# Kernel tuning notes

Hardware: AMD Instinct MI355X
Metric: run time of the kernel (lower is better)

Reference implementation:

```python
import jax, jax.numpy as jnp
import numpy as np
import math

B, S, D, H = 1, 4096, 1024, 16
DH = D // H


def setup_inputs() -> dict:
    key = jax.random.key(0)
    k1, k2, k3 = jax.random.split(key, 3)
    x = jax.random.normal(k1, (B, S, D), dtype=jnp.float32)
    # additive causal mask: 0 where allowed, -1e9 where masked (future)
    causal = jnp.tril(jnp.ones((S, S), dtype=bool))
    mask = jnp.where(causal, 0.0, -1e9).astype(jnp.float32)[None]  # [1,S,S]
    W_attn = jax.random.normal(k2, (D, 3 * D), dtype=jnp.float32) * 0.02
    b_attn = jnp.zeros((3 * D,), dtype=jnp.float32)
    W_proj = jax.random.normal(k3, (D, D), dtype=jnp.float32) * 0.02
    b_proj = jnp.zeros((D,), dtype=jnp.float32)
    return {"x": x, "mask": mask, "W_attn": W_attn, "b_attn": b_attn,
            "W_proj": W_proj, "b_proj": b_proj}


def reference(x, mask, W_attn, b_attn, W_proj, b_proj):
    # c_attn: fused QKV projection
    qkv = x @ W_attn + b_attn                      # [B,S,3D]
    q, k, v = jnp.split(qkv, 3, axis=-1)           # each [B,S,D]

    def heads(t):  # [B,S,D] -> [B,H,S,DH]
        return t.reshape(B, S, H, DH).transpose(0, 2, 1, 3)

    q, k, v = heads(q), heads(k), heads(v)
    # scores: eager O(S^2) matrix as in original
    w = jnp.einsum('bhqd,bhkd->bhqk', q, k) / math.sqrt(DH)
    w = w + mask[:, None, :, :]                    # broadcast over heads
    w = jax.nn.softmax(w, axis=-1)                 # dropout p=0 -> identity
    a = jnp.einsum('bhqk,bhkd->bhqd', w, v)        # [B,H,S,DH]
    a = a.transpose(0, 2, 1, 3).reshape(B, S, D)   # merge heads
    return a @ W_proj + b_proj
```

## Files before the change

### kernel.cpp

```cpp
#include <hip/hip_runtime.h>

typedef _Float16 half8 __attribute__((ext_vector_type(8)));
typedef short short8 __attribute__((ext_vector_type(8)));
typedef float floatx4 __attribute__((ext_vector_type(4)));

static __device__ __forceinline__ float bf2f(unsigned short u) {
  union { unsigned int u; float f; } c; c.u = ((unsigned int)u) << 16; return c.f;
}
static __device__ __forceinline__ unsigned short f2bf(float f) {
  union { float f; unsigned int u; } c; c.f = f;
  return (unsigned short)((c.u + 0x7fffu + ((c.u >> 16) & 1u)) >> 16);
}
static __device__ __forceinline__ unsigned short f2h(float f) {
  union { _Float16 h; unsigned short u; } c; c.h = (_Float16)f; return c.u;
}
static __device__ __forceinline__ unsigned int cvtpk(float a, float b) {
  unsigned int r;
  asm("v_cvt_pk_bf16_f32 %0, %1, %2" : "=v"(r) : "v"(a), "v"(b));
  return r;
}

#define GL2LDS16(gsrc, ldst)                                                        \
  __builtin_amdgcn_global_load_lds(                                                 \
      (const __attribute__((address_space(1))) void*)(const void*)(gsrc),           \
      (__attribute__((address_space(3))) void*)(void*)(ldst), 16, 0, 0)

static __device__ __forceinline__ int dtype_bf16(const unsigned short* mask16) {
  return mask16[1] != 0;
}

__global__ __launch_bounds__(256) void k_prep(const void* __restrict__ x,
    const void* __restrict__ Wa, const void* __restrict__ Wp,
    const unsigned short* __restrict__ mask16, _Float16* __restrict__ xh,
    _Float16* __restrict__ WaT, _Float16* __restrict__ WpT) {
  __shared__ float tile[64 * 65];
  const int dt = dtype_bf16(mask16);
  const int bx = blockIdx.x;
  const int tid = threadIdx.x;
  if (bx < 4096) {
    const int i = (bx * 256 + tid) * 4;
    _Float16 o[4];
    if (dt) {
      ushort4 u = *((const ushort4*)((const unsigned short*)x + i));
      o[0] = (_Float16)bf2f(u.x); o[1] = (_Float16)bf2f(u.y);
      o[2] = (_Float16)bf2f(u.z); o[3] = (_Float16)bf2f(u.w);
    } else {
      float4 f = *((const float4*)((const float*)x + i));
      o[0] = (_Float16)f.x; o[1] = (_Float16)f.y;
      o[2] = (_Float16)f.z; o[3] = (_Float16)f.w;
    }
    union { _Float16 h[4]; uint2 u; } pk;
    pk.h[0] = o[0]; pk.h[1] = o[1]; pk.h[2] = o[2]; pk.h[3] = o[3];
    *((uint2*)(xh + i)) = pk.u;
    return;
  }
  const void* in; _Float16* out; int n0, k0, N;
  if (bx < 4864) { const int b = bx - 4096; in = Wa; out = WaT; N = 3072;
                   n0 = (b % 48) * 64; k0 = (b / 48) * 64; }
  else           { const int b = bx - 4864; in = Wp; out = WpT; N = 1024;
                   n0 = (b % 16) * 64; k0 = (b / 16) * 64; }
  const int r = tid >> 2;
#pragma unroll
  for (int it = 0; it < 4; ++it) {
    const int c4 = (tid & 3) + it * 4;
    const size_t src = (size_t)(k0 + r) * N + n0 + c4 * 4;
    float v[4];
    if (dt) {
      ushort4 u = *((const ushort4*)((const unsigned short*)in + src));
      v[0] = bf2f(u.x); v[1] = bf2f(u.y); v[2] = bf2f(u.z); v[3] = bf2f(u.w);
    } else {
      float4 f = *((const float4*)((const float*)in + src));
      v[0] = f.x; v[1] = f.y; v[2] = f.z; v[3] = f.w;
    }
#pragma unroll
    for (int jj = 0; jj < 4; ++jj) tile[r * 65 + c4 * 4 + jj] = v[jj];
  }
  __syncthreads();
#pragma unroll
  for (int it = 0; it < 4; ++it) {
    const int rn = (tid >> 4) + it * 16;
    const int kc = tid & 15;
    union { _Float16 h[4]; uint2 u; } pk;
#pragma unroll
    for (int jj = 0; jj < 4; ++jj)
      pk.h[jj] = (_Float16)tile[(kc * 4 + jj) * 65 + rn];
    *(uint2*)(out + (size_t)(n0 + rn) * 1024 + k0 + kc * 4) = pk.u;
  }
}

template <int KD>
static __device__ __forceinline__ void gemm_mainloop(const _Float16* __restrict__ A,
    const _Float16* __restrict__ Bt, int m0, int n0,
    _Float16* As, _Float16* Bs, floatx4 acc[4][4]) {
  const int tid = threadIdx.x;
  const int wave = tid >> 6, lane = tid & 63;
  const int lq = lane & 15, quad = lane >> 4;
  const int wm = (wave >> 1) * 64, wn = (wave & 1) * 64;
  const int scol = (lane & 3) * 8;
  for (int k0 = 0; k0 < KD; k0 += 32) {
    __syncthreads();
#pragma unroll
    for (int op = 0; op < 2; ++op) {
      const int rbase = wave * 32 + op * 16;
      const int row = rbase + (lane >> 2);
      GL2LDS16(A + (size_t)(m0 + row) * KD + k0 + scol, As + rbase * 32);
      GL2LDS16(Bt + (size_t)(n0 + row) * KD + k0 + scol, Bs + rbase * 32);
    }
    __builtin_amdgcn_s_waitcnt(0x0f70);
    __syncthreads();
    half8 af[4], bf[4];
#pragma unroll
    for (int i = 0; i < 4; ++i) {
      af[i] = *(const half8*)(As + (wm + i * 16 + lq) * 32 + quad * 8);
      bf[i] = *(const half8*)(Bs + (wn + i * 16 + lq) * 32 + quad * 8);
    }
#pragma unroll
    for (int i = 0; i < 4; ++i)
#pragma unroll
      for (int j = 0; j < 4; ++j)
        acc[i][j] = __builtin_amdgcn_mfma_f32_16x16x32_f16(af[i], bf[j], acc[i][j], 0, 0, 0);
  }
}

__global__ __launch_bounds__(256, 1) void k_gemm_qkv(const _Float16* __restrict__ A,
    const _Float16* __restrict__ Bt, const void* __restrict__ bias,
    const unsigned short* __restrict__ mask16, _Float16* __restrict__ Qb,
    _Float16* __restrict__ Kb, unsigned short* __restrict__ VTb) {
  __shared__ __attribute__((aligned(16))) unsigned short smem[128 * 136];
  _Float16* As = (_Float16*)smem;
  _Float16* Bs = As + 4096;
  const int tid = threadIdx.x, wave = tid >> 6, lane = tid & 63;
  const int lq = lane & 15, quad = lane >> 4;
  const int m0 = blockIdx.y * 128, n0 = blockIdx.x * 128;
  const int wm = (wave >> 1) * 64, wn = (wave & 1) * 64;
  floatx4 acc[4][4] = {};
  gemm_mainloop<1024>(A, Bt, m0, n0, As, Bs, acc);
  const int dt = dtype_bf16(mask16);
  const int sec = n0 >> 10;
  const float scale = (sec == 0) ? 0.1803368801f : 1.0f;
  __syncthreads();
#pragma unroll
  for (int i = 0; i < 4; ++i) {
    const int lmb = wm + i * 16 + quad * 4;
#pragma unroll
    for (int j = 0; j < 4; ++j) {
      const int ln = wn + j * 16 + lq;
      const int gcol = n0 + ln;
      const float bv = dt ? bf2f(((const unsigned short*)bias)[gcol])
                          : ((const float*)bias)[gcol];
#pragma unroll
      for (int r = 0; r < 4; ++r) {
        const float v = (acc[i][j][r] + bv) * scale;
        const unsigned short bits = (sec == 2) ? f2bf(v) : f2h(v);
        if (sec == 2) smem[ln * 136 + lmb + r] = bits;
        else          smem[(lmb + r) * 136 + ln] = bits;
      }
    }
  }
  __syncthreads();
  if (sec == 2) {
#pragma unroll
    for (int it = 0; it < 8; ++it) {
      const int row = (tid >> 4) + it * 16;
      const int ch = tid & 15;
      const uint4 v = *(const uint4*)&smem[row * 136 + ch * 8];
      *(uint4*)(VTb + (size_t)(n0 + row - 2048) * 4096 + m0 + ch * 8) = v;
    }
  } else {
    _Float16* dst = (sec == 0) ? Qb : Kb;
#pragma unroll
    for (int it = 0; it < 8; ++it) {
      const int row = (tid >> 4) + it * 16;
      const int ch = tid & 15;
      const uint4 v = *(const uint4*)&smem[row * 136 + ch * 8];
      const int c = (n0 & 1023) + ch * 8;
      const int hh = c >> 6, dh = c & 63;
      *(uint4*)(dst + ((size_t)(hh * 4096 + m0 + row)) * 64 + dh) = v;
    }
  }
}

__global__ __launch_bounds__(256, 2) void k_attn(const _Float16* __restrict__ Qb,
    const _Float16* __restrict__ Kb, const unsigned short* __restrict__ VTb,
    unsigned short* __restrict__ Op0, unsigned short* __restrict__ Op1,
    unsigned short* __restrict__ Op2, unsigned short* __restrict__ Op3,
    float* __restrict__ Lp) {
  constexpr int S = 4096;
  const int bx = blockIdx.x;
  const int h  = bx & 15;
  const int pr = (bx >> 4) & 7;
  const int cj = bx >> 7;
  const int kbg = 15 - pr;
  const int ksm = pr;
  const int sB  = 64 - 4 * pr;
  const int fb  = sB / 17;
  const int p0 = cj * 17, p1 = p0 + 17;
  const int tid = threadIdx.x, wave = tid >> 6, lane = tid & 63;
  const int lq = lane & 15, quad = lane >> 4;
  __shared__ __attribute__((aligned(16))) _Float16 Ks[64 * 72];
  __shared__ __attribute__((aligned(16))) unsigned short VTs[64 * 72];
  const _Float16* Qh = Qb + (size_t)h * S * 64;
  const _Float16* Kh = Kb + (size_t)h * S * 64;
  const unsigned short* VTh = VTb + (size_t)h * 64 * S;
  short8 aones;
#pragma unroll
  for (int jj = 0; jj < 8; ++jj) aones[jj] = (short)0x3F80;
  const int srow = tid >> 2, schunk = (tid & 3) * 16;

#define LOADQ()                                                                     \
  {                                                                                 \
    const int qb0 = 256 * ku + wave * 64;                                           \
    _Pragma("unroll")                                                               \
    for (int m = 0; m < 4; ++m)                                                     \
      _Pragma("unroll")                                                             \
      for (int ch = 0; ch < 2; ++ch)                                                \
        qf[m][ch] = *(const half8*)(Qh + (size_t)(qb0 + m * 16 + lq) * 64           \
                                    + ch * 32 + quad * 8);                          \
  }
#define ZEROACC()                                                                   \
  {                                                                                 \
    _Pragma("unroll")                                                               \
    for (int nf = 0; nf < 4; ++nf)                                                  \
      _Pragma("unroll")                                                             \
      for (int m = 0; m < 4; ++m) o[nf][m] = (floatx4){0.f, 0.f, 0.f, 0.f};         \
    _Pragma("unroll")                                                               \
    for (int m = 0; m < 4; ++m) ol[m] = (floatx4){0.f, 0.f, 0.f, 0.f};              \
  }
#define EPILOGUE(SLOT)                                                              \
  {                                                                                 \
    const int sl = (SLOT);                                                          \
    unsigned short* Ob = sl == 0 ? Op0 : sl == 1 ? Op1 : sl == 2 ? Op2 : Op3;       \
    const int r0 = sl << 10;                                                        \
    const int qb0 = 256 * ku + wave * 64;                                           \
    _Pragma("unroll")                                                               \
    for (int m = 0; m < 4; ++m) {                                                   \
      const int q = qb0 + m * 16 + lq;                                              \
      _Pragma("unroll")                                                             \
      for (int nf = 0; nf < 4; ++nf) {                                              \
        union { unsigned short u[4]; uint2 v; } pk;                                 \
        _Pragma("unroll")                                                           \
        for (int r = 0; r < 4; ++r) pk.u[r] = f2bf(o[nf][m][r]);                    \
        *(uint2*)(Ob + (size_t)(q - r0) * 1024 + h * 64 + nf * 16 + quad * 4) =     \
            pk.v;                                                                   \
      }                                                                             \
      if (quad == 0) Lp[sl * 65536 + h * 4096 + q] = ol[m][0];                      \
    }                                                                               \
  }

  int ku = (p0 < sB) ? kbg : ksm;
  half8 qf[4][2];
  floatx4 o[4][4];
  floatx4 ol[4];
  LOADQ();
  ZEROACC();
  uint4 kreg0, kreg1, vreg0, vreg1;
  {
    const int t0 = (p0 < sB) ? p0 : p0 - sB;
    const int kt = t0 * 64;
    kreg0 = *(const uint4*)(Kh + (size_t)(kt + srow) * 64 + schunk);
    kreg1 = *(const uint4*)(Kh + (size_t)(kt + srow) * 64 + schunk + 8);
    vreg0 = *(const uint4*)(VTh + (size_t)srow * S + kt + schunk);
    vreg1 = *(const uint4*)(VTh + (size_t)srow * S + kt + schunk + 8);
  }
  for (int pos = p0; pos < p1; ++pos) {
    if (pos == sB) {
      EPILOGUE(cj);
      ku = ksm;
      LOADQ();
      ZEROACC();
    }
    const int t = (pos < sB) ? pos : pos - sB;
    const int kt = t * 64;
    __syncthreads();
    *(uint4*)(Ks + srow * 72 + schunk) = kreg0;
    *(uint4*)(Ks + srow * 72 + schunk + 8) = kreg1;
    *(uint4*)(VTs + srow * 72 + schunk) = vreg0;
    *(uint4*)(VTs + srow * 72 + schunk + 8) = vreg1;
    __syncthreads();
    if (pos + 1 < p1) {
      const int nx = pos + 1;
      const int tn = (nx < sB) ? nx : nx - sB;
      const int kn = tn * 64;
      kreg0 = *(const uint4*)(Kh + (size_t)(kn + srow) * 64 + schunk);
      kreg1 = *(const uint4*)(Kh + (size_t)(kn + srow) * 64 + schunk + 8);
      vreg0 = *(const uint4*)(VTh + (size_t)srow * S + kn + schunk);
      vreg1 = *(const uint4*)(VTh + (size_t)srow * S + kn + schunk + 8);
    }
    const int qb0 = 256 * ku + wave * 64;
    if ((wave >= 2) || (t < 4 * ku + 2)) {
#pragma unroll
      for (int c = 0; c < 2; ++c) {
        floatx4 sc[4][2];
        {
          half8 kf0[2], kf1[2];
#pragma unroll
          for (int kb = 0; kb < 2; ++kb) {
            const int row = (c * 2 + kb) * 16 + lq;
            kf0[kb] = *(const half8*)(Ks + row * 72 + quad * 8);
            kf1[kb] = *(const half8*)(Ks + row * 72 + 32 + quad * 8);
          }
#pragma unroll
          for (int m = 0; m < 4; ++m)
#pragma unroll
            for (int kb = 0; kb < 2; ++kb) {
              floatx4 z = {0.f, 0.f, 0.f, 0.f};
              z = __builtin_amdgcn_mfma_f32_16x16x32_f16(kf0[kb], qf[m][0], z, 0, 0, 0);
              sc[m][kb] = __builtin_amdgcn_mfma_f32_16x16x32_f16(kf1[kb], qf[m][1], z, 0, 0, 0);
            }
        }
        short8 pf[4];
#pragma unroll
        for (int m = 0; m < 4; ++m) {
          unsigned int dw0, dw1, dw2, dw3;
          if (kt + c * 32 + 31 > qb0 + m * 16) {
            const int q = qb0 + m * 16 + lq;
            float pv0[4], pv1[4];
#pragma unroll
            for (int r = 0; r < 4; ++r) {
              const int key0 = kt + (c * 2 + 0) * 16 + quad * 4 + r;
              const int key1 = kt + (c * 2 + 1) * 16 + quad * 4 + r;
              const float e0 = __builtin_amdgcn_exp2f(sc[m][0][r]);
              const float e1 = __builtin_amdgcn_exp2f(sc[m][1][r]);
              pv0[r] = (key0 > q) ? 0.f : e0;
              pv1[r] = (key1 > q) ? 0.f : e1;
            }
            dw0 = cvtpk(pv0[0], pv0[1]); dw1 = cvtpk(pv0[2], pv0[3]);
            dw2 = cvtpk(pv1[0], pv1[1]); dw3 = cvtpk(pv1[2], pv1[3]);
          } else {
            float pv0[4], pv1[4];
#pragma unroll
            for (int r = 0; r < 4; ++r) {
              pv0[r] = __builtin_amdgcn_exp2f(sc[m][0][r]);
              pv1[r] = __builtin_amdgcn_exp2f(sc[m][1][r]);
            }
            dw0 = cvtpk(pv0[0], pv0[1]); dw1 = cvtpk(pv0[2], pv0[3]);
            dw2 = cvtpk(pv1[0], pv1[1]); dw3 = cvtpk(pv1[2], pv1[3]);
          }
          asm("v_permlane32_swap_b32 %0, %1" : "+v"(dw0), "+v"(dw2));
          asm("v_permlane32_swap_b32 %0, %1" : "+v"(dw1), "+v"(dw3));
          asm("v_permlane16_swap_b32 %0, %1" : "+v"(dw0), "+v"(dw2));
          asm("v_permlane16_swap_b32 %0, %1" : "+v"(dw1), "+v"(dw3));
          union { unsigned int d[4]; short8 s; } u;
          u.d[0] = dw0; u.d[1] = dw1; u.d[2] = dw2; u.d[3] = dw3;
          pf[m] = u.s;
        }
#pragma unroll
        for (int nf = 0; nf < 4; ++nf) {
          const short8 vfr = *(const short8*)(VTs + (nf * 16 + lq) * 72 + c * 32 + quad * 8);
#pragma unroll
          for (int m = 0; m < 4; ++m)
            o[nf][m] = __builtin_amdgcn_mfma_f32_16x16x32_bf16(vfr, pf[m], o[nf][m], 0, 0, 0);
        }
#pragma unroll
        for (int m = 0; m < 4; ++m)
          ol[m] = __builtin_amdgcn_mfma_f32_16x16x32_bf16(aones, pf[m], ol[m], 0, 0, 0);
      }
    }
  }
  EPILOGUE((p1 <= sB) ? cj : cj - fb);
#undef LOADQ
#undef ZEROACC
#undef EPILOGUE
}

__global__ __launch_bounds__(256) void k_merge(const unsigned short* __restrict__ Op0,
    const unsigned short* __restrict__ Op1, const unsigned short* __restrict__ Op2,
    const unsigned short* __restrict__ Op3, const float* __restrict__ Lp,
    _Float16* __restrict__ Ah) {
  const int row = blockIdx.x;
  const int c = threadIdx.x * 4;
  const int h = c >> 6;
  const int k = row >> 8;
  const int n = (k >= 8) ? (4 * k + 20) / 17 : 4 - (64 - 4 * k) / 17;
  float l = 0.f, v0 = 0.f, v1 = 0.f, v2 = 0.f, v3 = 0.f;
#pragma unroll
  for (int s = 0; s < 4; ++s) {
    if (s < n) {
      const unsigned short* Ob = s == 0 ? Op0 : s == 1 ? Op1 : s == 2 ? Op2 : Op3;
      l += Lp[s * 65536 + h * 4096 + row];
      const ushort4 a = *(const ushort4*)(Ob + (size_t)(row - (s << 10)) * 1024 + c);
      v0 += bf2f(a.x); v1 += bf2f(a.y); v2 += bf2f(a.z); v3 += bf2f(a.w);
    }
  }
  const float inv = __builtin_amdgcn_rcpf(l);
  union { _Float16 h4[4]; uint2 u; } pk;
  pk.h4[0] = (_Float16)(v0 * inv);
  pk.h4[1] = (_Float16)(v1 * inv);
  pk.h4[2] = (_Float16)(v2 * inv);
  pk.h4[3] = (_Float16)(v3 * inv);
  *(uint2*)(Ah + (size_t)row * 1024 + c) = pk.u;
}

__global__ __launch_bounds__(256, 1) void k_gemm_proj(const _Float16* __restrict__ A,
    const _Float16* __restrict__ Bt, const void* __restrict__ bias,
    const unsigned short* __restrict__ mask16, void* __restrict__ out) {
  __shared__ __attribute__((aligned(16))) _Float16 As[64 * 32];
  __shared__ __attribute__((aligned(16))) _Float16 Bs[128 * 32];
  const int tid = threadIdx.x, wave = tid >> 6, lane = tid & 63;
  const int lq = lane & 15, quad = lane >> 4;
  const int m0 = blockIdx.y * 64, n0 = blockIdx.x * 128;
  const int wm = (wave >> 1) * 32, wn = (wave & 1) * 64;
  const int scol = (lane & 3) * 8;
  floatx4 acc[2][4] = {};
  for (int k0 = 0; k0 < 1024; k0 += 32) {
    __syncthreads();
    {
      const int arow = wave * 16 + (lane >> 2);
      GL2LDS16(A + (size_t)(m0 + arow) * 1024 + k0 + scol, As + wave * 16 * 32);
#pragma unroll
      for (int op = 0; op < 2; ++op) {
        const int rbase = wave * 32 + op * 16;
        const int row = rbase + (lane >> 2);
        GL2LDS16(Bt + (size_t)(n0 + row) * 1024 + k0 + scol, Bs + rbase * 32);
      }
    }
    __builtin_amdgcn_s_waitcnt(0x0f70);
    __syncthreads();
    half8 af[2], bf[4];
#pragma unroll
    for (int i = 0; i < 2; ++i)
      af[i] = *(const half8*)(As + (wm + i * 16 + lq) * 32 + quad * 8);
#pragma unroll
    for (int j = 0; j < 4; ++j)
      bf[j] = *(const half8*)(Bs + (wn + j * 16 + lq) * 32 + quad * 8);
#pragma unroll
    for (int i = 0; i < 2; ++i)
#pragma unroll
      for (int j = 0; j < 4; ++j)
        acc[i][j] = __builtin_amdgcn_mfma_f32_16x16x32_f16(af[i], bf[j], acc[i][j], 0, 0, 0);
  }
  const int dt = dtype_bf16(mask16);
#pragma unroll
  for (int i = 0; i < 2; ++i) {
    const int growb = m0 + wm + i * 16 + quad * 4;
#pragma unroll
    for (int j = 0; j < 4; ++j) {
      const int gcol = n0 + wn + j * 16 + lq;
      const float bv = dt ? bf2f(((const unsigned short*)bias)[gcol])
                          : ((const float*)bias)[gcol];
#pragma unroll
      for (int r = 0; r < 4; ++r) {
        const float v = acc[i][j][r] + bv;
        if (dt) ((unsigned short*)out)[(size_t)(growb + r) * 1024 + gcol] = f2bf(v);
        else    ((float*)out)[(size_t)(growb + r) * 1024 + gcol] = v;
      }
    }
  }
}

extern "C" void kernel_launch(void* const* d_in, const int* in_sizes, int n_in,
                              void* d_out, int out_size, void* d_ws, size_t ws_size,
                              hipStream_t stream) {
  const void* x    = d_in[0];
  const unsigned short* mask16 = (const unsigned short*)d_in[1];
  const void* Wa   = d_in[2];
  const void* ba   = d_in[3];
  const void* Wp   = d_in[4];
  const void* bp   = d_in[5];
  char* ws = (char*)d_ws;
  _Float16* WpT       = (_Float16*)(ws + 0);
  _Float16* WaT       = (_Float16*)(ws + 2097152);
  float*    Lp        = (float*)   (ws + 2097152);
  unsigned short* Op2 = (unsigned short*)(ws + 3145728);
  _Float16* xh        = (_Float16*)(ws + 8388608);
  unsigned short* Op0 = (unsigned short*)(ws + 8388608);
  _Float16* Qb        = (_Float16*)(ws + 16777216);
  _Float16* Ah        = (_Float16*)(ws + 16777216);
  _Float16* Kb        = (_Float16*)(ws + 25165824);
  unsigned short* VTb = (unsigned short*)(ws + 33554432);
  unsigned short* Op1 = (unsigned short*)(ws + 41943040);
  unsigned short* Op3 = (unsigned short*)(ws + 48234496);

  k_prep<<<5120, 256, 0, stream>>>(x, Wa, Wp, mask16, xh, WaT, WpT);
  { dim3 g(24, 32); k_gemm_qkv<<<g, 256, 0, stream>>>(xh, WaT, ba, mask16, Qb, Kb, VTb); }
  k_attn<<<512, 256, 0, stream>>>(Qb, Kb, VTb, Op0, Op1, Op2, Op3, Lp);
  k_merge<<<4096, 256, 0, stream>>>(Op0, Op1, Op2, Op3, Lp, Ah);
  { dim3 g(8, 64);  k_gemm_proj<<<g, 256, 0, stream>>>(Ah, WpT, bp, mask16, d_out); }
}
```

Measured before the change: 240.6 us.

## Double-buffer K/V tiles via async global-to-LDS loads with XOR swizzle

Replaces the register-staged K/V prefetch (global load into registers, then LDS store between two barriers) with direct global_load_lds into a double-buffered LDS tile, so the next tile streams in while the current one is computed. Padding is replaced by an XOR swizzle to avoid bank conflicts, and s_setprio raises wave priority around the MFMA blocks. This removes one barrier per iteration and the register round-trip. In exchange it doubles LDS use, which may limit occupancy, and relies on a full vmcnt wait at the end of each iteration.

```diff
diff --git a/kernel.cpp b/kernel.cpp
--- a/kernel.cpp
+++ b/kernel.cpp
@@ -197,16 +197,30 @@
   const int p0 = cj * 17, p1 = p0 + 17;
   const int tid = threadIdx.x, wave = tid >> 6, lane = tid & 63;
   const int lq = lane & 15, quad = lane >> 4;
-  __shared__ __attribute__((aligned(16))) _Float16 Ks[64 * 72];
-  __shared__ __attribute__((aligned(16))) unsigned short VTs[64 * 72];
+  __shared__ __attribute__((aligned(16))) _Float16 Ks[2][64 * 64];
+  __shared__ __attribute__((aligned(16))) unsigned short VTs[2][64 * 64];
   const _Float16* Qh = Qb + (size_t)h * S * 64;
   const _Float16* Kh = Kb + (size_t)h * S * 64;
   const unsigned short* VTh = VTb + (size_t)h * 64 * S;
   short8 aones;
 #pragma unroll
   for (int jj = 0; jj < 8; ++jj) aones[jj] = (short)0x3F80;
-  const int srow = tid >> 2, schunk = (tid & 3) * 16;
-
+  const int srow8 = lane >> 3;
+  const int swch  = ((lane & 7) ^ srow8) * 8;
+  const int rowKV = wave * 16 + srow8;
+  const int sdst  = wave * 1024 + lane * 8;
+  const int xr = lq & 7;
+
+#define STAGE(BUF, KT)                                                              \
+  {                                                                                 \
+    _Pragma("unroll")                                                               \
+    for (int j = 0; j < 2; ++j) {                                                   \
+      GL2LDS16(Kh + (size_t)((KT) + rowKV + j * 8) * 64 + swch,                     \
+               &Ks[BUF][wave * 1024 + j * 512]);                                    \
+      GL2LDS16(VTh + (size_t)(rowKV + j * 8) * S + (KT) + swch,                     \
+               &VTs[BUF][wave * 1024 + j * 512]);                                   \
+    }                                                                               \
+  }
 #define LOADQ()                                                                     \
   {                                                                                 \
     const int qb0 = 256 * ku + wave * 64;                                           \
@@ -253,39 +267,29 @@
   floatx4 ol[4];
   LOADQ();
   ZEROACC();
-  uint4 kreg0, kreg1, vreg0, vreg1;
   {
     const int t0 = (p0 < sB) ? p0 : p0 - sB;
-    const int kt = t0 * 64;
-    kreg0 = *(const uint4*)(Kh + (size_t)(kt + srow) * 64 + schunk);
-    kreg1 = *(const uint4*)(Kh + (size_t)(kt + srow) * 64 + schunk + 8);
-    vreg0 = *(const uint4*)(VTh + (size_t)srow * S + kt + schunk);
-    vreg1 = *(const uint4*)(VTh + (size_t)srow * S + kt + schunk + 8);
-  }
+    STAGE(0, t0 * 64);
+  }
+  __builtin_amdgcn_s_waitcnt(0x0f70);
+  __syncthreads();
   for (int pos = p0; pos < p1; ++pos) {
+    const int b = (pos - p0) & 1;
     if (pos == sB) {
       EPILOGUE(cj);
       ku = ksm;
       LOADQ();
       ZEROACC();
     }
-    const int t = (pos < sB) ? pos : pos - sB;
-    const int kt = t * 64;
-    __syncthreads();
-    *(uint4*)(Ks + srow * 72 + schunk) = kreg0;
-    *(uint4*)(Ks + srow * 72 + schunk + 8) = kreg1;
-    *(uint4*)(VTs + srow * 72 + schunk) = vreg0;
-    *(uint4*)(VTs + srow * 72 + schunk + 8) = vreg1;
-    __syncthreads();
     if (pos + 1 < p1) {
       const int nx = pos + 1;
       const int tn = (nx < sB) ? nx : nx - sB;
-      const int kn = tn * 64;
-      kreg0 = *(const uint4*)(Kh + (size_t)(kn + srow) * 64 + schunk);
-      kreg1 = *(const uint4*)(Kh + (size_t)(kn + srow) * 64 + schunk + 8);
-      vreg0 = *(const uint4*)(VTh + (size_t)srow * S + kn + schunk);
-      vreg1 = *(const uint4*)(VTh + (size_t)srow * S + kn + schunk + 8);
-    }
+      STAGE(b ^ 1, tn * 64);
+    }
+    const int t = (pos < sB) ? pos : pos - sB;
+    const int kt = t * 64;
+    const _Float16* Ksb = &Ks[b][0];
+    const unsigned short* Vsb = &VTs[b][0];
     const int qb0 = 256 * ku + wave * 64;
     if ((wave >= 2) || (t < 4 * ku + 2)) {
 #pragma unroll
@@ -296,9 +300,10 @@
 #pragma unroll
           for (int kb = 0; kb < 2; ++kb) {
             const int row = (c * 2 + kb) * 16 + lq;
-            kf0[kb] = *(const half8*)(Ks + row * 72 + quad * 8);
-            kf1[kb] = *(const half8*)(Ks + row * 72 + 32 + quad * 8);
+            kf0[kb] = *(const half8*)(Ksb + row * 64 + ((quad ^ xr) << 3));
+            kf1[kb] = *(const half8*)(Ksb + row * 64 + (((quad | 4) ^ xr) << 3));
           }
+          __builtin_amdgcn_s_setprio(1);
 #pragma unroll
           for (int m = 0; m < 4; ++m)
 #pragma unroll
@@ -307,6 +312,7 @@
               z = __builtin_amdgcn_mfma_f32_16x16x32_f16(kf0[kb], qf[m][0], z, 0, 0, 0);
               sc[m][kb] = __builtin_amdgcn_mfma_f32_16x16x32_f16(kf1[kb], qf[m][1], z, 0, 0, 0);
             }
+          __builtin_amdgcn_s_setprio(0);
         }
         short8 pf[4];
 #pragma unroll
@@ -344,9 +350,11 @@
           u.d[0] = dw0; u.d[1] = dw1; u.d[2] = dw2; u.d[3] = dw3;
           pf[m] = u.s;
         }
+        __builtin_amdgcn_s_setprio(1);
 #pragma unroll
         for (int nf = 0; nf < 4; ++nf) {
-          const short8 vfr = *(const short8*)(VTs + (nf * 16 + lq) * 72 + c * 32 + quad * 8);
+          const short8 vfr = *(const short8*)(
+              Vsb + (nf * 16 + lq) * 64 + ((((c << 2) | quad) ^ xr) << 3));
 #pragma unroll
           for (int m = 0; m < 4; ++m)
             o[nf][m] = __builtin_amdgcn_mfma_f32_16x16x32_bf16(vfr, pf[m], o[nf][m], 0, 0, 0);
@@ -354,10 +362,14 @@
 #pragma unroll
         for (int m = 0; m < 4; ++m)
           ol[m] = __builtin_amdgcn_mfma_f32_16x16x32_bf16(aones, pf[m], ol[m], 0, 0, 0);
+        __builtin_amdgcn_s_setprio(0);
       }
     }
+    __builtin_amdgcn_s_waitcnt(0x0f70);
+    __syncthreads();
   }
   EPILOGUE((p1 <= sB) ? cj : cj - fb);
+#undef STAGE
 #undef LOADQ
 #undef ZEROACC
 #undef EPILOGUE
```

Result: no change. 244.1 us (+1.5%).

## Deepen GEMM K-tiles to 64 with XOR-swizzled LDS and XCD-aware block mapping

Applied to the files above, without the earlier changes.

Both GEMM kernels now stage 64-wide K slices per iteration instead of 32. This halves the number of barrier and wait round-trips per tile. LDS rows are XOR-swizzled by row to avoid bank conflicts on the wider 128-byte rows. Launch grids become 1-D, with block IDs remapped so blocks on the same XCD share M rows, aiming for better L2 reuse. The cost is a doubled LDS footprint and more fragment registers per iteration.

```diff
diff --git a/kernel.cpp b/kernel.cpp
--- a/kernel.cpp
+++ b/kernel.cpp
@@ -89,36 +89,41 @@
 }
 
 template <int KD>
-static __device__ __forceinline__ void gemm_mainloop(const _Float16* __restrict__ A,
+static __device__ __forceinline__ void gemm_mainloop64(const _Float16* __restrict__ A,
     const _Float16* __restrict__ Bt, int m0, int n0,
     _Float16* As, _Float16* Bs, floatx4 acc[4][4]) {
   const int tid = threadIdx.x;
   const int wave = tid >> 6, lane = tid & 63;
   const int lq = lane & 15, quad = lane >> 4;
   const int wm = (wave >> 1) * 64, wn = (wave & 1) * 64;
-  const int scol = (lane & 3) * 8;
-  for (int k0 = 0; k0 < KD; k0 += 32) {
+  const int srow8 = lane >> 3;
+  const int swch = ((lane & 7) ^ srow8) * 8;
+  const int xr = lq & 7;
+  for (int k0 = 0; k0 < KD; k0 += 64) {
     __syncthreads();
 #pragma unroll
-    for (int op = 0; op < 2; ++op) {
-      const int rbase = wave * 32 + op * 16;
-      const int row = rbase + (lane >> 2);
-      GL2LDS16(A + (size_t)(m0 + row) * KD + k0 + scol, As + rbase * 32);
-      GL2LDS16(Bt + (size_t)(n0 + row) * KD + k0 + scol, Bs + rbase * 32);
+    for (int op = 0; op < 4; ++op) {
+      const int rb = wave * 32 + op * 8;
+      GL2LDS16(A + (size_t)(m0 + rb + srow8) * KD + k0 + swch, As + rb * 64);
+      GL2LDS16(Bt + (size_t)(n0 + rb + srow8) * KD + k0 + swch, Bs + rb * 64);
     }
     __builtin_amdgcn_s_waitcnt(0x0f70);
     __syncthreads();
-    half8 af[4], bf[4];
-#pragma unroll
-    for (int i = 0; i < 4; ++i) {
-      af[i] = *(const half8*)(As + (wm + i * 16 + lq) * 32 + quad * 8);
-      bf[i] = *(const half8*)(Bs + (wn + i * 16 + lq) * 32 + quad * 8);
-    }
+    half8 af[4][2], bf[4][2];
 #pragma unroll
     for (int i = 0; i < 4; ++i)
 #pragma unroll
-      for (int j = 0; j < 4; ++j)
-        acc[i][j] = __builtin_amdgcn_mfma_f32_16x16x32_f16(af[i], bf[j], acc[i][j], 0, 0, 0);
+      for (int ks = 0; ks < 2; ++ks) {
+        af[i][ks] = *(const half8*)(As + (wm + i * 16 + lq) * 64 + (((ks * 4 + quad) ^ xr) << 3));
+        bf[i][ks] = *(const half8*)(Bs + (wn + i * 16 + lq) * 64 + (((ks * 4 + quad) ^ xr) << 3));
+      }
+#pragma unroll
+    for (int i = 0; i < 4; ++i)
+#pragma unroll
+      for (int j = 0; j < 4; ++j) {
+        acc[i][j] = __builtin_amdgcn_mfma_f32_16x16x32_f16(af[i][0], bf[j][0], acc[i][j], 0, 0, 0);
+        acc[i][j] = __builtin_amdgcn_mfma_f32_16x16x32_f16(af[i][1], bf[j][1], acc[i][j], 0, 0, 0);
+      }
   }
 }
 
@@ -128,13 +133,17 @@
     _Float16* __restrict__ Kb, unsigned short* __restrict__ VTb) {
   __shared__ __attribute__((aligned(16))) unsigned short smem[128 * 136];
   _Float16* As = (_Float16*)smem;
-  _Float16* Bs = As + 4096;
+  _Float16* Bs = As + 8192;
+  const int id = blockIdx.x;
+  const int xcd = id & 7, rr = id >> 3;
+  const int by = xcd * 4 + rr / 24;
+  const int bxn = rr % 24;
   const int tid = threadIdx.x, wave = tid >> 6, lane = tid & 63;
   const int lq = lane & 15, quad = lane >> 4;
-  const int m0 = blockIdx.y * 128, n0 = blockIdx.x * 128;
+  const int m0 = by * 128, n0 = bxn * 128;
   const int wm = (wave >> 1) * 64, wn = (wave & 1) * 64;
   floatx4 acc[4][4] = {};
-  gemm_mainloop<1024>(A, Bt, m0, n0, As, Bs, acc);
+  gemm_mainloop64<1024>(A, Bt, m0, n0, As, Bs, acc);
   const int dt = dtype_bf16(mask16);
   const int sec = n0 >> 10;
   const float scale = (sec == 0) ? 0.1803368801f : 1.0f;
@@ -394,40 +403,52 @@
 __global__ __launch_bounds__(256, 1) void k_gemm_proj(const _Float16* __restrict__ A,
     const _Float16* __restrict__ Bt, const void* __restrict__ bias,
     const unsigned short* __restrict__ mask16, void* __restrict__ out) {
-  __shared__ __attribute__((aligned(16))) _Float16 As[64 * 32];
-  __shared__ __attribute__((aligned(16))) _Float16 Bs[128 * 32];
+  __shared__ __attribute__((aligned(16))) _Float16 As[64 * 64];
+  __shared__ __attribute__((aligned(16))) _Float16 Bs[128 * 64];
+  const int id = blockIdx.x;
+  const int xcd = id & 7, rr = id >> 3;
+  const int by = xcd * 8 + rr / 8;
+  const int bxn = rr % 8;
   const int tid = threadIdx.x, wave = tid >> 6, lane = tid & 63;
   const int lq = lane & 15, quad = lane >> 4;
-  const int m0 = blockIdx.y * 64, n0 = blockIdx.x * 128;
+  const int m0 = by * 64, n0 = bxn * 128;
   const int wm = (wave >> 1) * 32, wn = (wave & 1) * 64;
-  const int scol = (lane & 3) * 8;
+  const int srow8 = lane >> 3;
+  const int swch = ((lane & 7) ^ srow8) * 8;
+  const int xr = lq & 7;
   floatx4 acc[2][4] = {};
-  for (int k0 = 0; k0 < 1024; k0 += 32) {
+  for (int k0 = 0; k0 < 1024; k0 += 64) {
     __syncthreads();
-    {
-      const int arow = wave * 16 + (lane >> 2);
-      GL2LDS16(A + (size_t)(m0 + arow) * 1024 + k0 + scol, As + wave * 16 * 32);
-#pragma unroll
-      for (int op = 0; op < 2; ++op) {
-        const int rbase = wave * 32 + op * 16;
-        const int row = rbase + (lane >> 2);
-        GL2LDS16(Bt + (size_t)(n0 + row) * 1024 + k0 + scol, Bs + rbase * 32);
-      }
+#pragma unroll
+    for (int op = 0; op < 2; ++op) {
+      const int rb = wave * 16 + op * 8;
+      GL2LDS16(A + (size_t)(m0 + rb + srow8) * 1024 + k0 + swch, As + rb * 64);
+    }
+#pragma unroll
+    for (int op = 0; op < 4; ++op) {
+      const int rb = wave * 32 + op * 8;
+      GL2LDS16(Bt + (size_t)(n0 + rb + srow8) * 1024 + k0 + swch, Bs + rb * 64);
     }
     __builtin_amdgcn_s_waitcnt(0x0f70);
     __syncthreads();
-    half8 af[2], bf[4];
+    half8 af[2][2], bf[4][2];
 #pragma unroll
     for (int i = 0; i < 2; ++i)
-      af[i] = *(const half8*)(As + (wm + i * 16 + lq) * 32 + quad * 8);
+#pragma unroll
+      for (int ks = 0; ks < 2; ++ks)
+        af[i][ks] = *(const half8*)(As + (wm + i * 16 + lq) * 64 + (((ks * 4 + quad) ^ xr) << 3));
 #pragma unroll
     for (int j = 0; j < 4; ++j)
-      bf[j] = *(const half8*)(Bs + (wn + j * 16 + lq) * 32 + quad * 8);
+#pragma unroll
+      for (int ks = 0; ks < 2; ++ks)
+        bf[j][ks] = *(const half8*)(Bs + (wn + j * 16 + lq) * 64 + (((ks * 4 + quad) ^ xr) << 3));
 #pragma unroll
     for (int i = 0; i < 2; ++i)
 #pragma unroll
-      for (int j = 0; j < 4; ++j)
-        acc[i][j] = __builtin_amdgcn_mfma_f32_16x16x32_f16(af[i], bf[j], acc[i][j], 0, 0, 0);
+      for (int j = 0; j < 4; ++j) {
+        acc[i][j] = __builtin_amdgcn_mfma_f32_16x16x32_f16(af[i][0], bf[j][0], acc[i][j], 0, 0, 0);
+        acc[i][j] = __builtin_amdgcn_mfma_f32_16x16x32_f16(af[i][1], bf[j][1], acc[i][j], 0, 0, 0);
+      }
   }
   const int dt = dtype_bf16(mask16);
 #pragma unroll
@@ -472,8 +493,8 @@
   unsigned short* Op3 = (unsigned short*)(ws + 48234496);
 
   k_prep<<<5120, 256, 0, stream>>>(x, Wa, Wp, mask16, xh, WaT, WpT);
-  { dim3 g(24, 32); k_gemm_qkv<<<g, 256, 0, stream>>>(xh, WaT, ba, mask16, Qb, Kb, VTb); }
+  k_gemm_qkv<<<768, 256, 0, stream>>>(xh, WaT, ba, mask16, Qb, Kb, VTb);
   k_attn<<<512, 256, 0, stream>>>(Qb, Kb, VTb, Op0, Op1, Op2, Op3, Lp);
   k_merge<<<4096, 256, 0, stream>>>(Op0, Op1, Op2, Op3, Lp, Ah);
-  { dim3 g(8, 64);  k_gemm_proj<<<g, 256, 0, stream>>>(Ah, WpT, bp, mask16, d_out); }
-}
+  k_gemm_proj<<<512, 256, 0, stream>>>(Ah, WpT, bp, mask16, d_out);
+}
```

Result: slower. 246.9 us (+2.6%).
